# Optimization experiments

Hardware: AMD Instinct MI355X
Metric: run time of the kernel (lower is better)

Reference implementation:

```python
import jax, jax.numpy as jnp
import numpy as np

N_NODES = 100000
N_EDGES = 3200000
IN_F, HID, OUT = 3, 32, 1
NEG_SLOPE = 0.2


def _glorot(key, shape):
    fan_in, fan_out = shape[0], shape[-1]
    lim = jnp.sqrt(6.0 / (fan_in + fan_out)).astype(jnp.float32)
    return jax.random.uniform(key, shape, jnp.float32, -lim, lim)


def setup_inputs() -> dict:
    key = jax.random.key(0)
    ks = jax.random.split(key, 12)
    x = jax.random.normal(ks[0], (N_NODES, IN_F), jnp.float32)
    edge_index = jax.random.randint(ks[1], (2, N_EDGES), 0, N_NODES, jnp.int32)
    return {
        "x": x,
        "edge_index": edge_index,
        "W1": _glorot(ks[2], (IN_F, HID)),
        "att_src1": _glorot(ks[3], (1, HID))[0],
        "att_dst1": _glorot(ks[4], (1, HID))[0],
        "b1": jnp.zeros((HID,), jnp.float32),
        "W2": _glorot(ks[5], (HID, HID)),
        "att_src2": _glorot(ks[6], (1, HID))[0],
        "att_dst2": _glorot(ks[7], (1, HID))[0],
        "b2": jnp.zeros((HID,), jnp.float32),
        "Wl": _glorot(ks[8], (HID, OUT)),
        "bl": jnp.zeros((OUT,), jnp.float32),
    }


def gat_layer(x, src, dst, W, att_src, att_dst, b):
    # h: [N, HID] dense transform
    h = x @ W
    # per-node attention halves (compute once per node, gather per edge)
    a_s = h @ att_src  # [N]
    a_d = h @ att_dst  # [N]
    logits = jax.nn.leaky_relu(a_s[src] + a_d[dst], NEG_SLOPE)  # [E+N]
    # segment-softmax over incoming edges of each dst node
    m = jax.ops.segment_max(logits, dst, num_segments=N_NODES)
    m = jnp.where(jnp.isfinite(m), m, 0.0)
    ex = jnp.exp(logits - m[dst])
    denom = jax.ops.segment_sum(ex, dst, num_segments=N_NODES)
    coef = ex / (denom[dst] + 1e-16)
    # weighted scatter-aggregate of source messages
    out = jax.ops.segment_sum(coef[:, None] * h[src], dst, num_segments=N_NODES)
    return out + b


def reference(x, edge_index, W1, att_src1, att_dst1, b1, W2, att_src2, att_dst2, b2, Wl, bl):
    # PyG GATConv default: add self-loops
    loops = jnp.arange(N_NODES, dtype=edge_index.dtype)
    src = jnp.concatenate([edge_index[0], loops])
    dst = jnp.concatenate([edge_index[1], loops])
    h = gat_layer(x, src, dst, W1, att_src1, att_dst1, b1)
    h = jax.nn.relu(h)  # dropout is identity in eval
    h = gat_layer(h, src, dst, W2, att_src2, att_dst2, b2)
    h = jax.nn.relu(h)
    return h @ Wl + bl
```

## Files before the change

kernel.cpp:

```cpp
#include <hip/hip_runtime.h>
#include <hip/hip_fp16.h>

#define HID 32
#define BN 131
#define NBPAD 768
#define BSTRIDE 4608
#define CHUNK 4096

__device__ __forceinline__ float lrelu(float x) { return x > 0.0f ? x : 0.2f * x; }


struct BinSM {
    int stage[CHUNK];
    unsigned short sbid[CHUNK];
    int lhist[NBPAD], lexcl[NBPAD], lbase[NBPAD], lcur[NBPAD];
    int arr[256];
};
struct AggSM {
    int2  lpair[BSTRIDE];
    int   lhist[256], lscan[256], lcur[256];
    float adT[BN];
};

template<int BLK>
__device__ __forceinline__ void binscatter_chunk(BinSM& S, int base,
        const int* __restrict__ src, const int* __restrict__ dst,
        int* __restrict__ cursor, unsigned int* __restrict__ packed,
        int NBr, int E)
{
    int t = threadIdx.x;
    for (int i = t; i < NBPAD; i += BLK) { S.lhist[i] = 0; S.lcur[i] = 0; }
    __syncthreads();
    int cnt = E - base; if (cnt > CHUNK) cnt = CHUNK;
    for (int i = t; i < cnt; i += BLK)
        atomicAdd(&S.lhist[dst[base + i] / BN], 1);
    __syncthreads();
    int b0 = 3 * t;
    int c0 = 0, c1 = 0, c2 = 0, s = 0;
    if (t < 256) {
        c0 = S.lhist[b0]; c1 = S.lhist[b0 + 1]; c2 = S.lhist[b0 + 2];
        s = c0 + c1 + c2;
        S.arr[t] = s;
    }
    __syncthreads();
    for (int o = 1; o < 256; o <<= 1) {
        int v = (t < 256 && t >= o) ? S.arr[t - o] : 0;
        __syncthreads();
        if (t < 256) S.arr[t] += v;
        __syncthreads();
    }
    if (t < 256) {
        int ex = S.arr[t] - s;
        int e0 = ex, e1 = ex + c0, e2 = ex + c0 + c1;
        S.lexcl[b0] = e0; S.lexcl[b0 + 1] = e1; S.lexcl[b0 + 2] = e2;
        for (int i = 0; i < c0; ++i) S.sbid[e0 + i] = (unsigned short)b0;
        for (int i = 0; i < c1; ++i) S.sbid[e1 + i] = (unsigned short)(b0 + 1);
        for (int i = 0; i < c2; ++i) S.sbid[e2 + i] = (unsigned short)(b0 + 2);
    }
    for (int b = t; b < NBr; b += BLK)
        if (S.lhist[b]) S.lbase[b] = b * BSTRIDE + atomicAdd(&cursor[b], S.lhist[b]);
    __syncthreads();
    for (int i = t; i < cnt; i += BLK) {
        int d = dst[base + i];
        int sv = src[base + i];
        int b = d / BN;
        int dl = d - b * BN;
        int idx = S.lexcl[b] + atomicAdd(&S.lcur[b], 1);
        S.stage[idx] = (int)((unsigned)sv | ((unsigned)dl << 17));
    }
    __syncthreads();
    for (int i = t; i < cnt; i += BLK) {
        int b = S.sbid[i];
        int gpos = S.lbase[b] + (i - S.lexcl[b]);
        if (gpos < (b + 1) * BSTRIDE)
            packed[gpos] = (unsigned)S.stage[i];
    }
}

template<int BLK>
__device__ __forceinline__ void build_csr_pair(int2* lpair, float* adT,
        int* lhist, int* lscan, int* lcur,
        const unsigned int* __restrict__ pk, int cnt,
        const float* __restrict__ a_s, const float* __restrict__ a_d,
        int nodeBase, int N)
{
    int t = threadIdx.x;
    if (t < 256) { lhist[t] = 0; lcur[t] = 0; }
    if (t < BN) { int n = nodeBase + t; adT[t] = (n < N) ? a_d[n] : 0.0f; }
    __syncthreads();
    for (int i = t; i < cnt; i += BLK)
        atomicAdd(&lhist[(pk[i] >> 17) & 255], 1);
    __syncthreads();
    if (t < 256) lscan[t] = lhist[t];
    __syncthreads();
    for (int o = 1; o < 256; o <<= 1) {
        int v = (t < 256 && t >= o) ? lscan[t - o] : 0;
        __syncthreads();
        if (t < 256) lscan[t] += v;
        __syncthreads();
    }
    for (int i = t; i < cnt; i += BLK) {
        unsigned p = pk[i];
        int dl = (p >> 17) & 255;
        int sv = (int)(p & 0x1FFFF);
        float e = __expf(lrelu(a_s[sv] + adT[dl]));
        int pos = atomicAdd(&lcur[dl], 1);
        lpair[(lscan[dl] - lhist[dl]) + pos] = make_int2((int)p, __float_as_int(e));
    }
    __syncthreads();
}

__device__ __forceinline__ void agg_node(const __half* __restrict__ hh,
                                         float ex_self, const float* __restrict__ b,
                                         int n, int f,
                                         const int2* lpair,
                                         int off, int dg, float& vx, float& vy)
{
    float den = ex_self;
    float2 hs = __half22float2(*(const __half2*)(hh + (size_t)n * HID + 2 * f));
    float accx = ex_self * hs.x;
    float accy = ex_self * hs.y;
    int j = 0;
    for (; j + 8 <= dg; j += 8) {
        int2 p0 = lpair[off + j + 0], p1 = lpair[off + j + 1];
        int2 p2 = lpair[off + j + 2], p3 = lpair[off + j + 3];
        int2 p4 = lpair[off + j + 4], p5 = lpair[off + j + 5];
        int2 p6 = lpair[off + j + 6], p7 = lpair[off + j + 7];
        int s0 = p0.x & 0x1FFFF, s1 = p1.x & 0x1FFFF;
        int s2 = p2.x & 0x1FFFF, s3 = p3.x & 0x1FFFF;
        int s4 = p4.x & 0x1FFFF, s5 = p5.x & 0x1FFFF;
        int s6 = p6.x & 0x1FFFF, s7 = p7.x & 0x1FFFF;
        __half2 h0 = *(const __half2*)(hh + (size_t)s0 * HID + 2 * f);
        __half2 h1 = *(const __half2*)(hh + (size_t)s1 * HID + 2 * f);
        __half2 h2 = *(const __half2*)(hh + (size_t)s2 * HID + 2 * f);
        __half2 h3 = *(const __half2*)(hh + (size_t)s3 * HID + 2 * f);
        __half2 h4 = *(const __half2*)(hh + (size_t)s4 * HID + 2 * f);
        __half2 h5 = *(const __half2*)(hh + (size_t)s5 * HID + 2 * f);
        __half2 h6 = *(const __half2*)(hh + (size_t)s6 * HID + 2 * f);
        __half2 h7 = *(const __half2*)(hh + (size_t)s7 * HID + 2 * f);
        float e0 = __int_as_float(p0.y), e1 = __int_as_float(p1.y);
        float e2 = __int_as_float(p2.y), e3 = __int_as_float(p3.y);
        float e4 = __int_as_float(p4.y), e5 = __int_as_float(p5.y);
        float e6 = __int_as_float(p6.y), e7 = __int_as_float(p7.y);
        float2 q0 = __half22float2(h0), q1 = __half22float2(h1);
        float2 q2 = __half22float2(h2), q3 = __half22float2(h3);
        float2 q4 = __half22float2(h4), q5 = __half22float2(h5);
        float2 q6 = __half22float2(h6), q7 = __half22float2(h7);
        den += ((e0 + e1) + (e2 + e3)) + ((e4 + e5) + (e6 + e7));
        accx = fmaf(e0, q0.x, accx); accy = fmaf(e0, q0.y, accy);
        accx = fmaf(e1, q1.x, accx); accy = fmaf(e1, q1.y, accy);
        accx = fmaf(e2, q2.x, accx); accy = fmaf(e2, q2.y, accy);
        accx = fmaf(e3, q3.x, accx); accy = fmaf(e3, q3.y, accy);
        accx = fmaf(e4, q4.x, accx); accy = fmaf(e4, q4.y, accy);
        accx = fmaf(e5, q5.x, accx); accy = fmaf(e5, q5.y, accy);
        accx = fmaf(e6, q6.x, accx); accy = fmaf(e6, q6.y, accy);
        accx = fmaf(e7, q7.x, accx); accy = fmaf(e7, q7.y, accy);
    }
    for (; j < dg; ++j) {
        int2 p0 = lpair[off + j];
        int s0 = p0.x & 0x1FFFF;
        float e0 = __int_as_float(p0.y);
        float2 q0 = __half22float2(*(const __half2*)(hh + (size_t)s0 * HID + 2 * f));
        den += e0;
        accx = fmaf(e0, q0.x, accx);
        accy = fmaf(e0, q0.y, accy);
    }
    float inv = 1.0f / (den + 1e-16f);
    vx = fmaxf(accx * inv + b[2 * f], 0.0f);
    vy = fmaxf(accy * inv + b[2 * f + 1], 0.0f);
}

__device__ __forceinline__ void epi_mid(int n, int f, float vx, float vy,
        const float* __restrict__ W2, const float* __restrict__ as2w,
        const float* __restrict__ ad2w,
        __half* __restrict__ hh_out, float* __restrict__ as_out,
        float* __restrict__ ad_out)
{
    float hx = 0.0f, hy = 0.0f;
    #pragma unroll
    for (int k = 0; k < 16; ++k) {
        float va = __shfl(vx, k, 16);
        float vb = __shfl(vy, k, 16);
        float2 w0 = *(const float2*)(W2 + (2 * k) * HID + 2 * f);
        float2 w1 = *(const float2*)(W2 + (2 * k + 1) * HID + 2 * f);
        hx = fmaf(va, w0.x, hx); hy = fmaf(va, w0.y, hy);
        hx = fmaf(vb, w1.x, hx); hy = fmaf(vb, w1.y, hy);
    }
    *(__half2*)(hh_out + (size_t)n * HID + 2 * f) = __floats2half2_rn(hx, hy);
    float as = hx * as2w[2 * f] + hy * as2w[2 * f + 1];
    float ad = hx * ad2w[2 * f] + hy * ad2w[2 * f + 1];
    #pragma unroll
    for (int m2 = 8; m2 >= 1; m2 >>= 1) {
        as += __shfl_xor(as, m2, 16);
        ad += __shfl_xor(ad, m2, 16);
    }
    if (f == 0) { as_out[n] = as; ad_out[n] = ad; }
}


__global__ void k_transform1(const float* __restrict__ x,
                             const float* __restrict__ W1,
                             const float* __restrict__ att_src,
                             const float* __restrict__ att_dst,
                             __half* __restrict__ hh,
                             float* __restrict__ a_s,
                             float* __restrict__ a_d,
                             int* __restrict__ cursor, int N)
{
    int tid = blockIdx.x * blockDim.x + threadIdx.x;
    if (tid < NBPAD) cursor[tid] = 0;
    int n = tid >> 5, f = tid & 31;
    if (n >= N) return;
    float x0 = x[n * 3 + 0], x1 = x[n * 3 + 1], x2 = x[n * 3 + 2];
    float hv = x0 * W1[f] + x1 * W1[HID + f] + x2 * W1[2 * HID + f];
    hh[(size_t)n * HID + f] = __float2half(hv);
    float as = hv * att_src[f];
    float ad = hv * att_dst[f];
    #pragma unroll
    for (int m = 16; m >= 1; m >>= 1) {
        as += __shfl_xor(as, m, 32);
        ad += __shfl_xor(ad, m, 32);
    }
    if (f == 0) { a_s[n] = as; a_d[n] = ad; }
}

__global__ void __launch_bounds__(512) k_binscatter(const int* __restrict__ src,
        const int* __restrict__ dst, int* __restrict__ cursor,
        unsigned int* __restrict__ packed, int NBr, int E)
{
    __shared__ BinSM S;
    binscatter_chunk<512>(S, blockIdx.x * CHUNK, src, dst, cursor, packed, NBr, E);
}

__global__ void __launch_bounds__(512) k_agg_mid_f(const __half* __restrict__ hh,
        const float* __restrict__ a_s, const float* __restrict__ a_d,
        const int* __restrict__ cursor, const unsigned int* __restrict__ packed,
        const float* __restrict__ b1, const float* __restrict__ W2,
        const float* __restrict__ as2w, const float* __restrict__ ad2w,
        __half* __restrict__ hh_out, float* __restrict__ as_out,
        float* __restrict__ ad_out, int N)
{
    __shared__ AggSM S;
    int bk = blockIdx.x, t = threadIdx.x;
    int cnt = cursor[bk]; if (cnt > BSTRIDE) cnt = BSTRIDE;
    build_csr_pair<512>(S.lpair, S.adT, S.lhist, S.lscan, S.lcur,
                        packed + (size_t)bk * BSTRIDE, cnt, a_s, a_d, bk * BN, N);
    int g = t >> 4, f = t & 15;
    for (int dl = g; dl < BN; dl += 32) {
        int n = bk * BN + dl;
        if (n >= N) continue;
        int off = S.lscan[dl] - S.lhist[dl];
        int dg = S.lhist[dl];
        float exs = __expf(lrelu(a_s[n] + S.adT[dl]));
        float vx, vy;
        agg_node(hh, exs, b1, n, f, S.lpair, off, dg, vx, vy);
        epi_mid(n, f, vx, vy, W2, as2w, ad2w, hh_out, as_out, ad_out);
    }
}

__global__ void __launch_bounds__(512) k_agg_out_f(const __half* __restrict__ hh,
        const float* __restrict__ a_s, const float* __restrict__ a_d,
        const int* __restrict__ cursor, const unsigned int* __restrict__ packed,
        const float* __restrict__ b2, const float* __restrict__ Wl,
        const float* __restrict__ bl, float* __restrict__ out, int N)
{
    __shared__ AggSM S;
    int bk = blockIdx.x, t = threadIdx.x;
    int cnt = cursor[bk]; if (cnt > BSTRIDE) cnt = BSTRIDE;
    build_csr_pair<512>(S.lpair, S.adT, S.lhist, S.lscan, S.lcur,
                        packed + (size_t)bk * BSTRIDE, cnt, a_s, a_d, bk * BN, N);
    int g = t >> 4, f = t & 15;
    for (int dl = g; dl < BN; dl += 32) {
        int n = bk * BN + dl;
        if (n >= N) continue;
        int off = S.lscan[dl] - S.lhist[dl];
        int dg = S.lhist[dl];
        float exs = __expf(lrelu(a_s[n] + S.adT[dl]));
        float vx, vy;
        agg_node(hh, exs, b2, n, f, S.lpair, off, dg, vx, vy);
        float y = vx * Wl[2 * f] + vy * Wl[2 * f + 1];
        #pragma unroll
        for (int m2 = 8; m2 >= 1; m2 >>= 1)
            y += __shfl_xor(y, m2, 16);
        if (f == 0) out[n] = y + bl[0];
    }
}

extern "C" void kernel_launch(void* const* d_in, const int* in_sizes, int n_in,
                              void* d_out, int out_size, void* d_ws, size_t ws_size,
                              hipStream_t stream)
{
    const float* x        = (const float*)d_in[0];
    const int*   eidx     = (const int*)d_in[1];
    const float* W1       = (const float*)d_in[2];
    const float* att_src1 = (const float*)d_in[3];
    const float* att_dst1 = (const float*)d_in[4];
    const float* b1       = (const float*)d_in[5];
    const float* W2       = (const float*)d_in[6];
    const float* att_src2 = (const float*)d_in[7];
    const float* att_dst2 = (const float*)d_in[8];
    const float* b2       = (const float*)d_in[9];
    const float* Wl       = (const float*)d_in[10];
    const float* bl       = (const float*)d_in[11];
    float* out = (float*)d_out;

    int N = in_sizes[0] / 3;
    int E = in_sizes[1] / 2;
    const int* src = eidx;
    const int* dst = eidx + E;
    int NBr = (N + BN - 1) / BN;

    size_t szNHh = (size_t)N * HID * 2;
    size_t szN4  = (size_t)N * 4;
    size_t szPK  = (size_t)NBr * BSTRIDE * 4;

    char* ws = (char*)d_ws;
    __half* h1h    = (__half*)ws; ws += szNHh;
    __half* h2h    = (__half*)ws; ws += szNHh;
    unsigned int* packed = (unsigned int*)ws; ws += szPK;
    float*  a_s1   = (float*)ws;  ws += szN4;
    float*  a_d1   = (float*)ws;  ws += szN4;
    float*  a_s2   = (float*)ws;  ws += szN4;
    float*  a_d2   = (float*)ws;  ws += szN4;
    int*    cursor = (int*)ws;    ws += NBPAD * 4;

    const int B = 256;
    int gridNode32 = (N * HID + B - 1) / B;
    int gridBin    = (E + CHUNK - 1) / CHUNK;

    k_transform1<<<gridNode32, B, 0, stream>>>(x, W1, att_src1, att_dst1,
                                               h1h, a_s1, a_d1, cursor, N);
    k_binscatter<<<gridBin, 512, 0, stream>>>(src, dst, cursor, packed, NBr, E);
    k_agg_mid_f<<<NBr, 512, 0, stream>>>(h1h, a_s1, a_d1, cursor, packed,
                                         b1, W2, att_src2, att_dst2,
                                         h2h, a_s2, a_d2, N);
    k_agg_out_f<<<NBr, 512, 0, stream>>>(h2h, a_s2, a_d2, cursor, packed,
                                         b2, Wl, bl, out, N);
}
```

Measured before the change: 246.4 us.

## Presort edge bins once per dst node and widen aggregation to four features

A new k_sort kernel sorts each bin's packed edges by local destination once and writes per-node offset/degree metadata. Both aggregation passes then only compute edge weights in stream order, with no per-kernel histogram and scan. Bins shrink to 64 nodes with 256-thread blocks, and each thread handles four features using 8-byte half loads. This adds one launch and a global read/write pass over the packed edges in exchange for less repeated shared-memory work and higher occupancy.

```diff
diff --git a/kernel.cpp b/kernel.cpp
--- a/kernel.cpp
+++ b/kernel.cpp
@@ -2,200 +2,14 @@
 #include <hip/hip_fp16.h>
 
 #define HID 32
-#define BN 131
-#define NBPAD 768
-#define BSTRIDE 4608
+#define BN 64
+#define NBPAD 1792
+#define BSTRIDE 2432
 #define CHUNK 4096
+#define EPT 8
+#define SPT 10
 
 __device__ __forceinline__ float lrelu(float x) { return x > 0.0f ? x : 0.2f * x; }
-
-
-struct BinSM {
-    int stage[CHUNK];
-    unsigned short sbid[CHUNK];
-    int lhist[NBPAD], lexcl[NBPAD], lbase[NBPAD], lcur[NBPAD];
-    int arr[256];
-};
-struct AggSM {
-    int2  lpair[BSTRIDE];
-    int   lhist[256], lscan[256], lcur[256];
-    float adT[BN];
-};
-
-template<int BLK>
-__device__ __forceinline__ void binscatter_chunk(BinSM& S, int base,
-        const int* __restrict__ src, const int* __restrict__ dst,
-        int* __restrict__ cursor, unsigned int* __restrict__ packed,
-        int NBr, int E)
-{
-    int t = threadIdx.x;
-    for (int i = t; i < NBPAD; i += BLK) { S.lhist[i] = 0; S.lcur[i] = 0; }
-    __syncthreads();
-    int cnt = E - base; if (cnt > CHUNK) cnt = CHUNK;
-    for (int i = t; i < cnt; i += BLK)
-        atomicAdd(&S.lhist[dst[base + i] / BN], 1);
-    __syncthreads();
-    int b0 = 3 * t;
-    int c0 = 0, c1 = 0, c2 = 0, s = 0;
-    if (t < 256) {
-        c0 = S.lhist[b0]; c1 = S.lhist[b0 + 1]; c2 = S.lhist[b0 + 2];
-        s = c0 + c1 + c2;
-        S.arr[t] = s;
-    }
-    __syncthreads();
-    for (int o = 1; o < 256; o <<= 1) {
-        int v = (t < 256 && t >= o) ? S.arr[t - o] : 0;
-        __syncthreads();
-        if (t < 256) S.arr[t] += v;
-        __syncthreads();
-    }
-    if (t < 256) {
-        int ex = S.arr[t] - s;
-        int e0 = ex, e1 = ex + c0, e2 = ex + c0 + c1;
-        S.lexcl[b0] = e0; S.lexcl[b0 + 1] = e1; S.lexcl[b0 + 2] = e2;
-        for (int i = 0; i < c0; ++i) S.sbid[e0 + i] = (unsigned short)b0;
-        for (int i = 0; i < c1; ++i) S.sbid[e1 + i] = (unsigned short)(b0 + 1);
-        for (int i = 0; i < c2; ++i) S.sbid[e2 + i] = (unsigned short)(b0 + 2);
-    }
-    for (int b = t; b < NBr; b += BLK)
-        if (S.lhist[b]) S.lbase[b] = b * BSTRIDE + atomicAdd(&cursor[b], S.lhist[b]);
-    __syncthreads();
-    for (int i = t; i < cnt; i += BLK) {
-        int d = dst[base + i];
-        int sv = src[base + i];
-        int b = d / BN;
-        int dl = d - b * BN;
-        int idx = S.lexcl[b] + atomicAdd(&S.lcur[b], 1);
-        S.stage[idx] = (int)((unsigned)sv | ((unsigned)dl << 17));
-    }
-    __syncthreads();
-    for (int i = t; i < cnt; i += BLK) {
-        int b = S.sbid[i];
-        int gpos = S.lbase[b] + (i - S.lexcl[b]);
-        if (gpos < (b + 1) * BSTRIDE)
-            packed[gpos] = (unsigned)S.stage[i];
-    }
-}
-
-template<int BLK>
-__device__ __forceinline__ void build_csr_pair(int2* lpair, float* adT,
-        int* lhist, int* lscan, int* lcur,
-        const unsigned int* __restrict__ pk, int cnt,
-        const float* __restrict__ a_s, const float* __restrict__ a_d,
-        int nodeBase, int N)
-{
-    int t = threadIdx.x;
-    if (t < 256) { lhist[t] = 0; lcur[t] = 0; }
-    if (t < BN) { int n = nodeBase + t; adT[t] = (n < N) ? a_d[n] : 0.0f; }
-    __syncthreads();
-    for (int i = t; i < cnt; i += BLK)
-        atomicAdd(&lhist[(pk[i] >> 17) & 255], 1);
-    __syncthreads();
-    if (t < 256) lscan[t] = lhist[t];
-    __syncthreads();
-    for (int o = 1; o < 256; o <<= 1) {
-        int v = (t < 256 && t >= o) ? lscan[t - o] : 0;
-        __syncthreads();
-        if (t < 256) lscan[t] += v;
-        __syncthreads();
-    }
-    for (int i = t; i < cnt; i += BLK) {
-        unsigned p = pk[i];
-        int dl = (p >> 17) & 255;
-        int sv = (int)(p & 0x1FFFF);
-        float e = __expf(lrelu(a_s[sv] + adT[dl]));
-        int pos = atomicAdd(&lcur[dl], 1);
-        lpair[(lscan[dl] - lhist[dl]) + pos] = make_int2((int)p, __float_as_int(e));
-    }
-    __syncthreads();
-}
-
-__device__ __forceinline__ void agg_node(const __half* __restrict__ hh,
-                                         float ex_self, const float* __restrict__ b,
-                                         int n, int f,
-                                         const int2* lpair,
-                                         int off, int dg, float& vx, float& vy)
-{
-    float den = ex_self;
-    float2 hs = __half22float2(*(const __half2*)(hh + (size_t)n * HID + 2 * f));
-    float accx = ex_self * hs.x;
-    float accy = ex_self * hs.y;
-    int j = 0;
-    for (; j + 8 <= dg; j += 8) {
-        int2 p0 = lpair[off + j + 0], p1 = lpair[off + j + 1];
-        int2 p2 = lpair[off + j + 2], p3 = lpair[off + j + 3];
-        int2 p4 = lpair[off + j + 4], p5 = lpair[off + j + 5];
-        int2 p6 = lpair[off + j + 6], p7 = lpair[off + j + 7];
-        int s0 = p0.x & 0x1FFFF, s1 = p1.x & 0x1FFFF;
-        int s2 = p2.x & 0x1FFFF, s3 = p3.x & 0x1FFFF;
-        int s4 = p4.x & 0x1FFFF, s5 = p5.x & 0x1FFFF;
-        int s6 = p6.x & 0x1FFFF, s7 = p7.x & 0x1FFFF;
-        __half2 h0 = *(const __half2*)(hh + (size_t)s0 * HID + 2 * f);
-        __half2 h1 = *(const __half2*)(hh + (size_t)s1 * HID + 2 * f);
-        __half2 h2 = *(const __half2*)(hh + (size_t)s2 * HID + 2 * f);
-        __half2 h3 = *(const __half2*)(hh + (size_t)s3 * HID + 2 * f);
-        __half2 h4 = *(const __half2*)(hh + (size_t)s4 * HID + 2 * f);
-        __half2 h5 = *(const __half2*)(hh + (size_t)s5 * HID + 2 * f);
-        __half2 h6 = *(const __half2*)(hh + (size_t)s6 * HID + 2 * f);
-        __half2 h7 = *(const __half2*)(hh + (size_t)s7 * HID + 2 * f);
-        float e0 = __int_as_float(p0.y), e1 = __int_as_float(p1.y);
-        float e2 = __int_as_float(p2.y), e3 = __int_as_float(p3.y);
-        float e4 = __int_as_float(p4.y), e5 = __int_as_float(p5.y);
-        float e6 = __int_as_float(p6.y), e7 = __int_as_float(p7.y);
-        float2 q0 = __half22float2(h0), q1 = __half22float2(h1);
-        float2 q2 = __half22float2(h2), q3 = __half22float2(h3);
-        float2 q4 = __half22float2(h4), q5 = __half22float2(h5);
-        float2 q6 = __half22float2(h6), q7 = __half22float2(h7);
-        den += ((e0 + e1) + (e2 + e3)) + ((e4 + e5) + (e6 + e7));
-        accx = fmaf(e0, q0.x, accx); accy = fmaf(e0, q0.y, accy);
-        accx = fmaf(e1, q1.x, accx); accy = fmaf(e1, q1.y, accy);
-        accx = fmaf(e2, q2.x, accx); accy = fmaf(e2, q2.y, accy);
-        accx = fmaf(e3, q3.x, accx); accy = fmaf(e3, q3.y, accy);
-        accx = fmaf(e4, q4.x, accx); accy = fmaf(e4, q4.y, accy);
-        accx = fmaf(e5, q5.x, accx); accy = fmaf(e5, q5.y, accy);
-        accx = fmaf(e6, q6.x, accx); accy = fmaf(e6, q6.y, accy);
-        accx = fmaf(e7, q7.x, accx); accy = fmaf(e7, q7.y, accy);
-    }
-    for (; j < dg; ++j) {
-        int2 p0 = lpair[off + j];
-        int s0 = p0.x & 0x1FFFF;
-        float e0 = __int_as_float(p0.y);
-        float2 q0 = __half22float2(*(const __half2*)(hh + (size_t)s0 * HID + 2 * f));
-        den += e0;
-        accx = fmaf(e0, q0.x, accx);
-        accy = fmaf(e0, q0.y, accy);
-    }
-    float inv = 1.0f / (den + 1e-16f);
-    vx = fmaxf(accx * inv + b[2 * f], 0.0f);
-    vy = fmaxf(accy * inv + b[2 * f + 1], 0.0f);
-}
-
-__device__ __forceinline__ void epi_mid(int n, int f, float vx, float vy,
-        const float* __restrict__ W2, const float* __restrict__ as2w,
-        const float* __restrict__ ad2w,
-        __half* __restrict__ hh_out, float* __restrict__ as_out,
-        float* __restrict__ ad_out)
-{
-    float hx = 0.0f, hy = 0.0f;
-    #pragma unroll
-    for (int k = 0; k < 16; ++k) {
-        float va = __shfl(vx, k, 16);
-        float vb = __shfl(vy, k, 16);
-        float2 w0 = *(const float2*)(W2 + (2 * k) * HID + 2 * f);
-        float2 w1 = *(const float2*)(W2 + (2 * k + 1) * HID + 2 * f);
-        hx = fmaf(va, w0.x, hx); hy = fmaf(va, w0.y, hy);
-        hx = fmaf(vb, w1.x, hx); hy = fmaf(vb, w1.y, hy);
-    }
-    *(__half2*)(hh_out + (size_t)n * HID + 2 * f) = __floats2half2_rn(hx, hy);
-    float as = hx * as2w[2 * f] + hy * as2w[2 * f + 1];
-    float ad = hx * ad2w[2 * f] + hy * ad2w[2 * f + 1];
-    #pragma unroll
-    for (int m2 = 8; m2 >= 1; m2 >>= 1) {
-        as += __shfl_xor(as, m2, 16);
-        ad += __shfl_xor(ad, m2, 16);
-    }
-    if (f == 0) { as_out[n] = as; ad_out[n] = ad; }
-}
 
 
 __global__ void k_transform1(const float* __restrict__ x,
@@ -224,17 +38,274 @@
     if (f == 0) { a_s[n] = as; a_d[n] = ad; }
 }
 
+
 __global__ void __launch_bounds__(512) k_binscatter(const int* __restrict__ src,
         const int* __restrict__ dst, int* __restrict__ cursor,
-        unsigned int* __restrict__ packed, int NBr, int E)
-{
-    __shared__ BinSM S;
-    binscatter_chunk<512>(S, blockIdx.x * CHUNK, src, dst, cursor, packed, NBr, E);
-}
-
-__global__ void __launch_bounds__(512) k_agg_mid_f(const __half* __restrict__ hh,
+        unsigned int* __restrict__ packed, int E)
+{
+    __shared__ int stage[CHUNK];
+    __shared__ unsigned short sbid[CHUNK];
+    __shared__ int lidx[NBPAD];
+    __shared__ int lbase[NBPAD];
+    __shared__ int arr[256];
+
+    int t = threadIdx.x;
+    int base = blockIdx.x * CHUNK;
+    int cnt = E - base; if (cnt > CHUNK) cnt = CHUNK;
+
+    for (int i = t; i < NBPAD; i += 512) lidx[i] = 0;
+    __syncthreads();
+
+    int myb[EPT]; unsigned mypk[EPT];
+    #pragma unroll
+    for (int u = 0; u < EPT; ++u) {
+        int i = t + u * 512;
+        myb[u] = -1;
+        if (i < cnt) {
+            int d = dst[base + i];
+            int s = src[base + i];
+            int b = d >> 6;
+            myb[u] = b;
+            mypk[u] = (unsigned)s | ((unsigned)(d & 63) << 17);
+            atomicAdd(&lidx[b], 1);
+        }
+    }
+    __syncthreads();
+
+    int c[7]; int ssum = 0; int b0 = 7 * t;
+    if (t < 256) {
+        #pragma unroll
+        for (int k = 0; k < 7; ++k) { c[k] = lidx[b0 + k]; ssum += c[k]; }
+        arr[t] = ssum;
+    }
+    __syncthreads();
+    for (int o = 1; o < 256; o <<= 1) {
+        int v = (t < 256 && t >= o) ? arr[t - o] : 0;
+        __syncthreads();
+        if (t < 256) arr[t] += v;
+        __syncthreads();
+    }
+    if (t < 256) {
+        int run = arr[t] - ssum;
+        #pragma unroll
+        for (int k = 0; k < 7; ++k) {
+            int ck = c[k];
+            lidx[b0 + k] = run;
+            if (ck) {
+                int gb = (b0 + k) * BSTRIDE + atomicAdd(&cursor[b0 + k], ck);
+                lbase[b0 + k] = gb - run;
+                for (int i2 = 0; i2 < ck; ++i2)
+                    sbid[run + i2] = (unsigned short)(b0 + k);
+            }
+            run += ck;
+        }
+    }
+    __syncthreads();
+
+    #pragma unroll
+    for (int u = 0; u < EPT; ++u) {
+        if (myb[u] >= 0) {
+            int idx = atomicAdd(&lidx[myb[u]], 1);
+            stage[idx] = (int)mypk[u];
+        }
+    }
+    __syncthreads();
+
+    for (int i = t; i < cnt; i += 512) {
+        int b = sbid[i];
+        int gpos = lbase[b] + i;
+        if (gpos < (b + 1) * BSTRIDE) packed[gpos] = (unsigned)stage[i];
+    }
+}
+
+
+__global__ void __launch_bounds__(256) k_sort(const int* __restrict__ cursor,
+        unsigned int* __restrict__ packed, int* __restrict__ nmeta, int N)
+{
+    __shared__ int hist[64];
+    __shared__ int scn[64];
+    __shared__ int stage[BSTRIDE];
+
+    int bk = blockIdx.x, t = threadIdx.x;
+    int cnt = cursor[bk]; if (cnt > BSTRIDE) cnt = BSTRIDE;
+    if (t < 64) hist[t] = 0;
+    __syncthreads();
+
+    unsigned pk[SPT];
+    #pragma unroll
+    for (int u = 0; u < SPT; ++u) {
+        int i = t + u * 256;
+        if (i < cnt) {
+            pk[u] = packed[(size_t)bk * BSTRIDE + i];
+            atomicAdd(&hist[(pk[u] >> 17) & 63], 1);
+        }
+    }
+    __syncthreads();
+
+    if (t < 64) scn[t] = hist[t];
+    __syncthreads();
+    for (int o = 1; o < 64; o <<= 1) {
+        int v = (t < 64 && t >= o) ? scn[t - o] : 0;
+        __syncthreads();
+        if (t < 64) scn[t] += v;
+        __syncthreads();
+    }
+    if (t < 64) {
+        int cdeg = hist[t];
+        int ex = scn[t] - cdeg;
+        hist[t] = ex;
+        int n = bk * BN + t;
+        if (n < N) nmeta[n] = ex | (cdeg << 16);
+    }
+    __syncthreads();
+
+    #pragma unroll
+    for (int u = 0; u < SPT; ++u) {
+        int i = t + u * 256;
+        if (i < cnt) {
+            int idx = atomicAdd(&hist[(pk[u] >> 17) & 63], 1);
+            stage[idx] = (int)pk[u];
+        }
+    }
+    __syncthreads();
+
+    for (int i = t; i < cnt; i += 256)
+        packed[(size_t)bk * BSTRIDE + i] = (unsigned)stage[i];
+}
+
+
+struct AggSM {
+    int2  lpair[BSTRIDE];
+    float adT[BN];
+    float asT[BN];
+    int   meta[BN];
+};
+
+template<int BLK>
+__device__ __forceinline__ void build_stream(AggSM& S,
+        const unsigned int* __restrict__ pk, int cnt,
+        const float* __restrict__ a_s, const float* __restrict__ a_d,
+        const int* __restrict__ nmeta, int nodeBase, int N)
+{
+    int t = threadIdx.x;
+    if (t < BN) {
+        int n = nodeBase + t;
+        bool ok = n < N;
+        S.meta[t] = ok ? nmeta[n] : 0;
+        S.adT[t]  = ok ? a_d[n] : 0.0f;
+        S.asT[t]  = ok ? a_s[n] : 0.0f;
+    }
+    __syncthreads();
+    #pragma unroll
+    for (int u = 0; u < SPT; ++u) {
+        int i = t + u * BLK;
+        if (i < cnt) {
+            unsigned p = pk[i];
+            int sv = (int)(p & 0x1FFFF);
+            int dl = (p >> 17) & 63;
+            float e = __expf(lrelu(a_s[sv] + S.adT[dl]));
+            S.lpair[i] = make_int2(sv, __float_as_int(e));
+        }
+    }
+    __syncthreads();
+}
+
+__device__ __forceinline__ void agg_node8(const __half* __restrict__ hh,
+        float exs, const float* __restrict__ b, int n, int f,
+        const int2* lpair, int off, int dg,
+        float& v0, float& v1, float& v2, float& v3)
+{
+    uint2 us = *(const uint2*)(hh + (size_t)n * HID + 4 * f);
+    float2 s01 = __half22float2(*(__half2*)&us.x);
+    float2 s23 = __half22float2(*(__half2*)&us.y);
+    float den = exs;
+    float a0 = exs * s01.x, a1 = exs * s01.y, a2 = exs * s23.x, a3 = exs * s23.y;
+
+    int j = 0;
+    for (; j + 8 <= dg; j += 8) {
+        int2 p[8]; uint2 uu[8];
+        #pragma unroll
+        for (int q = 0; q < 8; ++q) p[q] = lpair[off + j + q];
+        #pragma unroll
+        for (int q = 0; q < 8; ++q)
+            uu[q] = *(const uint2*)(hh + (size_t)p[q].x * HID + 4 * f);
+        #pragma unroll
+        for (int q = 0; q < 8; ++q) {
+            float e = __int_as_float(p[q].y);
+            float2 qa = __half22float2(*(__half2*)&uu[q].x);
+            float2 qb = __half22float2(*(__half2*)&uu[q].y);
+            den += e;
+            a0 = fmaf(e, qa.x, a0); a1 = fmaf(e, qa.y, a1);
+            a2 = fmaf(e, qb.x, a2); a3 = fmaf(e, qb.y, a3);
+        }
+    }
+    for (; j < dg; ++j) {
+        int2 pp = lpair[off + j];
+        uint2 uu = *(const uint2*)(hh + (size_t)pp.x * HID + 4 * f);
+        float e = __int_as_float(pp.y);
+        float2 qa = __half22float2(*(__half2*)&uu.x);
+        float2 qb = __half22float2(*(__half2*)&uu.y);
+        den += e;
+        a0 = fmaf(e, qa.x, a0); a1 = fmaf(e, qa.y, a1);
+        a2 = fmaf(e, qb.x, a2); a3 = fmaf(e, qb.y, a3);
+    }
+    float inv = 1.0f / (den + 1e-16f);
+    float4 bb = *(const float4*)(b + 4 * f);
+    v0 = fmaxf(a0 * inv + bb.x, 0.0f);
+    v1 = fmaxf(a1 * inv + bb.y, 0.0f);
+    v2 = fmaxf(a2 * inv + bb.z, 0.0f);
+    v3 = fmaxf(a3 * inv + bb.w, 0.0f);
+}
+
+__device__ __forceinline__ void epi_mid8(int n, int f,
+        float v0, float v1, float v2, float v3,
+        const float* __restrict__ W2, const float* __restrict__ as2w,
+        const float* __restrict__ ad2w,
+        __half* __restrict__ hh_out, float* __restrict__ as_out,
+        float* __restrict__ ad_out)
+{
+    float h0 = 0.0f, h1 = 0.0f, h2 = 0.0f, h3 = 0.0f;
+    #pragma unroll
+    for (int k = 0; k < 8; ++k) {
+        float aa[4];
+        aa[0] = __shfl(v0, k, 8);
+        aa[1] = __shfl(v1, k, 8);
+        aa[2] = __shfl(v2, k, 8);
+        aa[3] = __shfl(v3, k, 8);
+        const float* wr = W2 + (4 * k) * HID + 4 * f;
+        #pragma unroll
+        for (int c = 0; c < 4; ++c) {
+            float4 w = *(const float4*)(wr + c * HID);
+            h0 = fmaf(aa[c], w.x, h0);
+            h1 = fmaf(aa[c], w.y, h1);
+            h2 = fmaf(aa[c], w.z, h2);
+            h3 = fmaf(aa[c], w.w, h3);
+        }
+    }
+    __half2 o01 = __floats2half2_rn(h0, h1);
+    __half2 o23 = __floats2half2_rn(h2, h3);
+    uint2 st;
+    st.x = *(unsigned*)&o01;
+    st.y = *(unsigned*)&o23;
+    *(uint2*)(hh_out + (size_t)n * HID + 4 * f) = st;
+
+    float4 asw = *(const float4*)(as2w + 4 * f);
+    float4 adw = *(const float4*)(ad2w + 4 * f);
+    float as = h0 * asw.x + h1 * asw.y + h2 * asw.z + h3 * asw.w;
+    float ad = h0 * adw.x + h1 * adw.y + h2 * adw.z + h3 * adw.w;
+    #pragma unroll
+    for (int m2 = 4; m2 >= 1; m2 >>= 1) {
+        as += __shfl_xor(as, m2, 8);
+        ad += __shfl_xor(ad, m2, 8);
+    }
+    if (f == 0) { as_out[n] = as; ad_out[n] = ad; }
+}
+
+
+__global__ void __launch_bounds__(256, 8) k_agg_mid(const __half* __restrict__ hh,
         const float* __restrict__ a_s, const float* __restrict__ a_d,
         const int* __restrict__ cursor, const unsigned int* __restrict__ packed,
+        const int* __restrict__ nmeta,
         const float* __restrict__ b1, const float* __restrict__ W2,
         const float* __restrict__ as2w, const float* __restrict__ ad2w,
         __half* __restrict__ hh_out, float* __restrict__ as_out,
@@ -243,48 +314,51 @@
     __shared__ AggSM S;
     int bk = blockIdx.x, t = threadIdx.x;
     int cnt = cursor[bk]; if (cnt > BSTRIDE) cnt = BSTRIDE;
-    build_csr_pair<512>(S.lpair, S.adT, S.lhist, S.lscan, S.lcur,
-                        packed + (size_t)bk * BSTRIDE, cnt, a_s, a_d, bk * BN, N);
-    int g = t >> 4, f = t & 15;
+    build_stream<256>(S, packed + (size_t)bk * BSTRIDE, cnt, a_s, a_d,
+                      nmeta, bk * BN, N);
+    int g = t >> 3, f = t & 7;
     for (int dl = g; dl < BN; dl += 32) {
         int n = bk * BN + dl;
         if (n >= N) continue;
-        int off = S.lscan[dl] - S.lhist[dl];
-        int dg = S.lhist[dl];
-        float exs = __expf(lrelu(a_s[n] + S.adT[dl]));
-        float vx, vy;
-        agg_node(hh, exs, b1, n, f, S.lpair, off, dg, vx, vy);
-        epi_mid(n, f, vx, vy, W2, as2w, ad2w, hh_out, as_out, ad_out);
-    }
-}
-
-__global__ void __launch_bounds__(512) k_agg_out_f(const __half* __restrict__ hh,
+        int m = S.meta[dl];
+        int off = m & 0xFFFF, dg = m >> 16;
+        float exs = __expf(lrelu(S.asT[dl] + S.adT[dl]));
+        float v0, v1, v2, v3;
+        agg_node8(hh, exs, b1, n, f, S.lpair, off, dg, v0, v1, v2, v3);
+        epi_mid8(n, f, v0, v1, v2, v3, W2, as2w, ad2w, hh_out, as_out, ad_out);
+    }
+}
+
+__global__ void __launch_bounds__(256, 8) k_agg_out(const __half* __restrict__ hh,
         const float* __restrict__ a_s, const float* __restrict__ a_d,
         const int* __restrict__ cursor, const unsigned int* __restrict__ packed,
+        const int* __restrict__ nmeta,
         const float* __restrict__ b2, const float* __restrict__ Wl,
         const float* __restrict__ bl, float* __restrict__ out, int N)
 {
     __shared__ AggSM S;
     int bk = blockIdx.x, t = threadIdx.x;
     int cnt = cursor[bk]; if (cnt > BSTRIDE) cnt = BSTRIDE;
-    build_csr_pair<512>(S.lpair, S.adT, S.lhist, S.lscan, S.lcur,
-                        packed + (size_t)bk * BSTRIDE, cnt, a_s, a_d, bk * BN, N);
-    int g = t >> 4, f = t & 15;
+    build_stream<256>(S, packed + (size_t)bk * BSTRIDE, cnt, a_s, a_d,
+                      nmeta, bk * BN, N);
+    int g = t >> 3, f = t & 7;
     for (int dl = g; dl < BN; dl += 32) {
         int n = bk * BN + dl;
         if (n >= N) continue;
-        int off = S.lscan[dl] - S.lhist[dl];
-        int dg = S.lhist[dl];
-        float exs = __expf(lrelu(a_s[n] + S.adT[dl]));
-        float vx, vy;
-        agg_node(hh, exs, b2, n, f, S.lpair, off, dg, vx, vy);
-        float y = vx * Wl[2 * f] + vy * Wl[2 * f + 1];
-        #pragma unroll
-        for (int m2 = 8; m2 >= 1; m2 >>= 1)
-            y += __shfl_xor(y, m2, 16);
+        int m = S.meta[dl];
+        int off = m & 0xFFFF, dg = m >> 16;
+        float exs = __expf(lrelu(S.asT[dl] + S.adT[dl]));
+        float v0, v1, v2, v3;
+        agg_node8(hh, exs, b2, n, f, S.lpair, off, dg, v0, v1, v2, v3);
+        float4 wl = *(const float4*)(Wl + 4 * f);
+        float y = v0 * wl.x + v1 * wl.y + v2 * wl.z + v3 * wl.w;
+        #pragma unroll
+        for (int m2 = 4; m2 >= 1; m2 >>= 1)
+            y += __shfl_xor(y, m2, 8);
         if (f == 0) out[n] = y + bl[0];
     }
 }
+
 
 extern "C" void kernel_launch(void* const* d_in, const int* in_sizes, int n_in,
                               void* d_out, int out_size, void* d_ws, size_t ws_size,
@@ -322,6 +396,7 @@
     float*  a_d1   = (float*)ws;  ws += szN4;
     float*  a_s2   = (float*)ws;  ws += szN4;
     float*  a_d2   = (float*)ws;  ws += szN4;
+    int*    nmeta  = (int*)ws;    ws += szN4;
     int*    cursor = (int*)ws;    ws += NBPAD * 4;
 
     const int B = 256;
@@ -330,10 +405,11 @@
 
     k_transform1<<<gridNode32, B, 0, stream>>>(x, W1, att_src1, att_dst1,
                                                h1h, a_s1, a_d1, cursor, N);
-    k_binscatter<<<gridBin, 512, 0, stream>>>(src, dst, cursor, packed, NBr, E);
-    k_agg_mid_f<<<NBr, 512, 0, stream>>>(h1h, a_s1, a_d1, cursor, packed,
-                                         b1, W2, att_src2, att_dst2,
-                                         h2h, a_s2, a_d2, N);
-    k_agg_out_f<<<NBr, 512, 0, stream>>>(h2h, a_s2, a_d2, cursor, packed,
-                                         b2, Wl, bl, out, N);
-}
+    k_binscatter<<<gridBin, 512, 0, stream>>>(src, dst, cursor, packed, E);
+    k_sort<<<NBr, 256, 0, stream>>>(cursor, packed, nmeta, N);
+    k_agg_mid<<<NBr, 256, 0, stream>>>(h1h, a_s1, a_d1, cursor, packed, nmeta,
+                                       b1, W2, att_src2, att_dst2,
+                                       h2h, a_s2, a_d2, N);
+    k_agg_out<<<NBr, 256, 0, stream>>>(h2h, a_s2, a_d2, cursor, packed, nmeta,
+                                       b2, Wl, bl, out, N);
+}
```

After: 322.4 us. 1.31x slower.

## Split aggregation bins across three blocks and register-cache binscatter edges

Applied to the files above, without the earlier changes.

Each aggregation block now handles a third of a destination bin, about 44 nodes, at 256 threads, with a much smaller shared CSR buffer. This raises occupancy and the number of blocks, but each block rescans the whole bin's packed edges and filters them, so the packed edge reads triple. The binscatter kernel uses larger chunks, keeps each thread's src/dst in registers instead of reading them twice, and pads the global cursors to avoid contention on shared cache lines. The lpair entries now store a plain source index, which removes the masking in the gather loop, and a capacity clamp (LPCAP) could drop edges for very high-degree slices.

```diff
diff --git a/kernel.cpp b/kernel.cpp
--- a/kernel.cpp
+++ b/kernel.cpp
@@ -5,9 +5,41 @@
 #define BN 131
 #define NBPAD 768
 #define BSTRIDE 4608
-#define CHUNK 4096
+#define CHUNK 6144
+#define EPT 12
+#define CPAD 16
+#define NSPLIT 3
+#define HNMAX 44
+#define LPCAP 1700
 
 __device__ __forceinline__ float lrelu(float x) { return x > 0.0f ? x : 0.2f * x; }
+
+
+__global__ void k_transform1(const float* __restrict__ x,
+                             const float* __restrict__ W1,
+                             const float* __restrict__ att_src,
+                             const float* __restrict__ att_dst,
+                             __half* __restrict__ hh,
+                             float* __restrict__ a_s,
+                             float* __restrict__ a_d,
+                             int* __restrict__ cursor, int N)
+{
+    int tid = blockIdx.x * blockDim.x + threadIdx.x;
+    if (tid < NBPAD * CPAD) cursor[tid] = 0;
+    int n = tid >> 5, f = tid & 31;
+    if (n >= N) return;
+    float x0 = x[n * 3 + 0], x1 = x[n * 3 + 1], x2 = x[n * 3 + 2];
+    float hv = x0 * W1[f] + x1 * W1[HID + f] + x2 * W1[2 * HID + f];
+    hh[(size_t)n * HID + f] = __float2half(hv);
+    float as = hv * att_src[f];
+    float ad = hv * att_dst[f];
+    #pragma unroll
+    for (int m = 16; m >= 1; m >>= 1) {
+        as += __shfl_xor(as, m, 32);
+        ad += __shfl_xor(ad, m, 32);
+    }
+    if (f == 0) { a_s[n] = as; a_d[n] = ad; }
+}
 
 
 struct BinSM {
@@ -16,25 +48,31 @@
     int lhist[NBPAD], lexcl[NBPAD], lbase[NBPAD], lcur[NBPAD];
     int arr[256];
 };
-struct AggSM {
-    int2  lpair[BSTRIDE];
-    int   lhist[256], lscan[256], lcur[256];
-    float adT[BN];
-};
-
-template<int BLK>
-__device__ __forceinline__ void binscatter_chunk(BinSM& S, int base,
-        const int* __restrict__ src, const int* __restrict__ dst,
-        int* __restrict__ cursor, unsigned int* __restrict__ packed,
-        int NBr, int E)
-{
+
+__global__ void __launch_bounds__(512) k_binscatter(const int* __restrict__ src,
+        const int* __restrict__ dst, int* __restrict__ cursor,
+        unsigned int* __restrict__ packed, int NBr, int E)
+{
+    __shared__ BinSM S;
     int t = threadIdx.x;
-    for (int i = t; i < NBPAD; i += BLK) { S.lhist[i] = 0; S.lcur[i] = 0; }
-    __syncthreads();
+    int base = blockIdx.x * CHUNK;
     int cnt = E - base; if (cnt > CHUNK) cnt = CHUNK;
-    for (int i = t; i < cnt; i += BLK)
-        atomicAdd(&S.lhist[dst[base + i] / BN], 1);
-    __syncthreads();
+
+    for (int i = t; i < NBPAD; i += 512) { S.lhist[i] = 0; S.lcur[i] = 0; }
+    __syncthreads();
+
+    int myd[EPT], mys[EPT];
+    #pragma unroll
+    for (int u = 0; u < EPT; ++u) {
+        int i = t + u * 512;
+        myd[u] = -1;
+        if (i < cnt) { myd[u] = dst[base + i]; mys[u] = src[base + i]; }
+    }
+    #pragma unroll
+    for (int u = 0; u < EPT; ++u)
+        if (myd[u] >= 0) atomicAdd(&S.lhist[myd[u] / BN], 1);
+    __syncthreads();
+
     int b0 = 3 * t;
     int c0 = 0, c1 = 0, c2 = 0, s = 0;
     if (t < 256) {
@@ -57,19 +95,24 @@
         for (int i = 0; i < c1; ++i) S.sbid[e1 + i] = (unsigned short)(b0 + 1);
         for (int i = 0; i < c2; ++i) S.sbid[e2 + i] = (unsigned short)(b0 + 2);
     }
-    for (int b = t; b < NBr; b += BLK)
-        if (S.lhist[b]) S.lbase[b] = b * BSTRIDE + atomicAdd(&cursor[b], S.lhist[b]);
-    __syncthreads();
-    for (int i = t; i < cnt; i += BLK) {
-        int d = dst[base + i];
-        int sv = src[base + i];
-        int b = d / BN;
-        int dl = d - b * BN;
-        int idx = S.lexcl[b] + atomicAdd(&S.lcur[b], 1);
-        S.stage[idx] = (int)((unsigned)sv | ((unsigned)dl << 17));
-    }
-    __syncthreads();
-    for (int i = t; i < cnt; i += BLK) {
+    for (int b = t; b < NBr; b += 512)
+        if (S.lhist[b])
+            S.lbase[b] = b * BSTRIDE + atomicAdd(&cursor[b * CPAD], S.lhist[b]);
+    __syncthreads();
+
+    #pragma unroll
+    for (int u = 0; u < EPT; ++u) {
+        if (myd[u] >= 0) {
+            int d = myd[u];
+            int b = d / BN;
+            int dl = d - b * BN;
+            int idx = S.lexcl[b] + atomicAdd(&S.lcur[b], 1);
+            S.stage[idx] = (int)((unsigned)mys[u] | ((unsigned)dl << 17));
+        }
+    }
+    __syncthreads();
+
+    for (int i = t; i < cnt; i += 512) {
         int b = S.sbid[i];
         int gpos = S.lbase[b] + (i - S.lexcl[b]);
         if (gpos < (b + 1) * BSTRIDE)
@@ -77,35 +120,45 @@
     }
 }
 
-template<int BLK>
-__device__ __forceinline__ void build_csr_pair(int2* lpair, float* adT,
-        int* lhist, int* lscan, int* lcur,
+
+struct AggSM {
+    int2  lpair[LPCAP];
+    int   hist[64], scn[64], cur[64];
+    float adT[HNMAX];
+};
+
+__device__ __forceinline__ void build_slice(AggSM& S,
         const unsigned int* __restrict__ pk, int cnt,
         const float* __restrict__ a_s, const float* __restrict__ a_d,
-        int nodeBase, int N)
+        int nodeBase, int dlo, int HN, int N)
 {
     int t = threadIdx.x;
-    if (t < 256) { lhist[t] = 0; lcur[t] = 0; }
-    if (t < BN) { int n = nodeBase + t; adT[t] = (n < N) ? a_d[n] : 0.0f; }
-    __syncthreads();
-    for (int i = t; i < cnt; i += BLK)
-        atomicAdd(&lhist[(pk[i] >> 17) & 255], 1);
-    __syncthreads();
-    if (t < 256) lscan[t] = lhist[t];
-    __syncthreads();
-    for (int o = 1; o < 256; o <<= 1) {
-        int v = (t < 256 && t >= o) ? lscan[t - o] : 0;
+    if (t < 64) { S.hist[t] = 0; S.cur[t] = 0; }
+    if (t < HN) { int n = nodeBase + dlo + t; S.adT[t] = (n < N) ? a_d[n] : 0.0f; }
+    __syncthreads();
+    for (int i = t; i < cnt; i += 256) {
+        unsigned ldl = ((pk[i] >> 17) & 255) - (unsigned)dlo;
+        if (ldl < (unsigned)HN) atomicAdd(&S.hist[ldl], 1);
+    }
+    __syncthreads();
+    if (t < 64) S.scn[t] = S.hist[t];
+    __syncthreads();
+    for (int o = 1; o < 64; o <<= 1) {
+        int v = (t < 64 && t >= o) ? S.scn[t - o] : 0;
         __syncthreads();
-        if (t < 256) lscan[t] += v;
+        if (t < 64) S.scn[t] += v;
         __syncthreads();
     }
-    for (int i = t; i < cnt; i += BLK) {
+    for (int i = t; i < cnt; i += 256) {
         unsigned p = pk[i];
-        int dl = (p >> 17) & 255;
-        int sv = (int)(p & 0x1FFFF);
-        float e = __expf(lrelu(a_s[sv] + adT[dl]));
-        int pos = atomicAdd(&lcur[dl], 1);
-        lpair[(lscan[dl] - lhist[dl]) + pos] = make_int2((int)p, __float_as_int(e));
+        unsigned ldl = ((p >> 17) & 255) - (unsigned)dlo;
+        if (ldl < (unsigned)HN) {
+            int sv = (int)(p & 0x1FFFF);
+            float e = __expf(lrelu(a_s[sv] + S.adT[ldl]));
+            int pos = atomicAdd(&S.cur[ldl], 1);
+            int idx = (S.scn[ldl] - S.hist[ldl]) + pos;
+            if (idx < LPCAP) S.lpair[idx] = make_int2(sv, __float_as_int(e));
+        }
     }
     __syncthreads();
 }
@@ -126,18 +179,14 @@
         int2 p2 = lpair[off + j + 2], p3 = lpair[off + j + 3];
         int2 p4 = lpair[off + j + 4], p5 = lpair[off + j + 5];
         int2 p6 = lpair[off + j + 6], p7 = lpair[off + j + 7];
-        int s0 = p0.x & 0x1FFFF, s1 = p1.x & 0x1FFFF;
-        int s2 = p2.x & 0x1FFFF, s3 = p3.x & 0x1FFFF;
-        int s4 = p4.x & 0x1FFFF, s5 = p5.x & 0x1FFFF;
-        int s6 = p6.x & 0x1FFFF, s7 = p7.x & 0x1FFFF;
-        __half2 h0 = *(const __half2*)(hh + (size_t)s0 * HID + 2 * f);
-        __half2 h1 = *(const __half2*)(hh + (size_t)s1 * HID + 2 * f);
-        __half2 h2 = *(const __half2*)(hh + (size_t)s2 * HID + 2 * f);
-        __half2 h3 = *(const __half2*)(hh + (size_t)s3 * HID + 2 * f);
-        __half2 h4 = *(const __half2*)(hh + (size_t)s4 * HID + 2 * f);
-        __half2 h5 = *(const __half2*)(hh + (size_t)s5 * HID + 2 * f);
-        __half2 h6 = *(const __half2*)(hh + (size_t)s6 * HID + 2 * f);
-        __half2 h7 = *(const __half2*)(hh + (size_t)s7 * HID + 2 * f);
+        __half2 h0 = *(const __half2*)(hh + (size_t)p0.x * HID + 2 * f);
+        __half2 h1 = *(const __half2*)(hh + (size_t)p1.x * HID + 2 * f);
+        __half2 h2 = *(const __half2*)(hh + (size_t)p2.x * HID + 2 * f);
+        __half2 h3 = *(const __half2*)(hh + (size_t)p3.x * HID + 2 * f);
+        __half2 h4 = *(const __half2*)(hh + (size_t)p4.x * HID + 2 * f);
+        __half2 h5 = *(const __half2*)(hh + (size_t)p5.x * HID + 2 * f);
+        __half2 h6 = *(const __half2*)(hh + (size_t)p6.x * HID + 2 * f);
+        __half2 h7 = *(const __half2*)(hh + (size_t)p7.x * HID + 2 * f);
         float e0 = __int_as_float(p0.y), e1 = __int_as_float(p1.y);
         float e2 = __int_as_float(p2.y), e3 = __int_as_float(p3.y);
         float e4 = __int_as_float(p4.y), e5 = __int_as_float(p5.y);
@@ -158,9 +207,8 @@
     }
     for (; j < dg; ++j) {
         int2 p0 = lpair[off + j];
-        int s0 = p0.x & 0x1FFFF;
         float e0 = __int_as_float(p0.y);
-        float2 q0 = __half22float2(*(const __half2*)(hh + (size_t)s0 * HID + 2 * f));
+        float2 q0 = __half22float2(*(const __half2*)(hh + (size_t)p0.x * HID + 2 * f));
         den += e0;
         accx = fmaf(e0, q0.x, accx);
         accy = fmaf(e0, q0.y, accy);
@@ -198,41 +246,7 @@
 }
 
 
-__global__ void k_transform1(const float* __restrict__ x,
-                             const float* __restrict__ W1,
-                             const float* __restrict__ att_src,
-                             const float* __restrict__ att_dst,
-                             __half* __restrict__ hh,
-                             float* __restrict__ a_s,
-                             float* __restrict__ a_d,
-                             int* __restrict__ cursor, int N)
-{
-    int tid = blockIdx.x * blockDim.x + threadIdx.x;
-    if (tid < NBPAD) cursor[tid] = 0;
-    int n = tid >> 5, f = tid & 31;
-    if (n >= N) return;
-    float x0 = x[n * 3 + 0], x1 = x[n * 3 + 1], x2 = x[n * 3 + 2];
-    float hv = x0 * W1[f] + x1 * W1[HID + f] + x2 * W1[2 * HID + f];
-    hh[(size_t)n * HID + f] = __float2half(hv);
-    float as = hv * att_src[f];
-    float ad = hv * att_dst[f];
-    #pragma unroll
-    for (int m = 16; m >= 1; m >>= 1) {
-        as += __shfl_xor(as, m, 32);
-        ad += __shfl_xor(ad, m, 32);
-    }
-    if (f == 0) { a_s[n] = as; a_d[n] = ad; }
-}
-
-__global__ void __launch_bounds__(512) k_binscatter(const int* __restrict__ src,
-        const int* __restrict__ dst, int* __restrict__ cursor,
-        unsigned int* __restrict__ packed, int NBr, int E)
-{
-    __shared__ BinSM S;
-    binscatter_chunk<512>(S, blockIdx.x * CHUNK, src, dst, cursor, packed, NBr, E);
-}
-
-__global__ void __launch_bounds__(512) k_agg_mid_f(const __half* __restrict__ hh,
+__global__ void __launch_bounds__(256, 8) k_agg_mid(const __half* __restrict__ hh,
         const float* __restrict__ a_s, const float* __restrict__ a_d,
         const int* __restrict__ cursor, const unsigned int* __restrict__ packed,
         const float* __restrict__ b1, const float* __restrict__ W2,
@@ -241,41 +255,47 @@
         float* __restrict__ ad_out, int N)
 {
     __shared__ AggSM S;
-    int bk = blockIdx.x, t = threadIdx.x;
-    int cnt = cursor[bk]; if (cnt > BSTRIDE) cnt = BSTRIDE;
-    build_csr_pair<512>(S.lpair, S.adT, S.lhist, S.lscan, S.lcur,
-                        packed + (size_t)bk * BSTRIDE, cnt, a_s, a_d, bk * BN, N);
+    int bid = blockIdx.x, t = threadIdx.x;
+    int bk = bid / NSPLIT, k = bid - NSPLIT * bk;
+    int dlo = k * HNMAX;
+    int HN = BN - dlo; if (HN > HNMAX) HN = HNMAX;
+    int cnt = cursor[bk * CPAD]; if (cnt > BSTRIDE) cnt = BSTRIDE;
+    build_slice(S, packed + (size_t)bk * BSTRIDE, cnt, a_s, a_d, bk * BN, dlo, HN, N);
     int g = t >> 4, f = t & 15;
-    for (int dl = g; dl < BN; dl += 32) {
-        int n = bk * BN + dl;
+    for (int ldl = g; ldl < HN; ldl += 16) {
+        int n = bk * BN + dlo + ldl;
         if (n >= N) continue;
-        int off = S.lscan[dl] - S.lhist[dl];
-        int dg = S.lhist[dl];
-        float exs = __expf(lrelu(a_s[n] + S.adT[dl]));
+        int off = S.scn[ldl] - S.hist[ldl];
+        int dg = S.hist[ldl];
+        if (off + dg > LPCAP) dg = LPCAP - off;
+        float exs = __expf(lrelu(a_s[n] + S.adT[ldl]));
         float vx, vy;
         agg_node(hh, exs, b1, n, f, S.lpair, off, dg, vx, vy);
         epi_mid(n, f, vx, vy, W2, as2w, ad2w, hh_out, as_out, ad_out);
     }
 }
 
-__global__ void __launch_bounds__(512) k_agg_out_f(const __half* __restrict__ hh,
+__global__ void __launch_bounds__(256, 8) k_agg_out(const __half* __restrict__ hh,
         const float* __restrict__ a_s, const float* __restrict__ a_d,
         const int* __restrict__ cursor, const unsigned int* __restrict__ packed,
         const float* __restrict__ b2, const float* __restrict__ Wl,
         const float* __restrict__ bl, float* __restrict__ out, int N)
 {
     __shared__ AggSM S;
-    int bk = blockIdx.x, t = threadIdx.x;
-    int cnt = cursor[bk]; if (cnt > BSTRIDE) cnt = BSTRIDE;
-    build_csr_pair<512>(S.lpair, S.adT, S.lhist, S.lscan, S.lcur,
-                        packed + (size_t)bk * BSTRIDE, cnt, a_s, a_d, bk * BN, N);
+    int bid = blockIdx.x, t = threadIdx.x;
+    int bk = bid / NSPLIT, k = bid - NSPLIT * bk;
+    int dlo = k * HNMAX;
+    int HN = BN - dlo; if (HN > HNMAX) HN = HNMAX;
+    int cnt = cursor[bk * CPAD]; if (cnt > BSTRIDE) cnt = BSTRIDE;
+    build_slice(S, packed + (size_t)bk * BSTRIDE, cnt, a_s, a_d, bk * BN, dlo, HN, N);
     int g = t >> 4, f = t & 15;
-    for (int dl = g; dl < BN; dl += 32) {
-        int n = bk * BN + dl;
+    for (int ldl = g; ldl < HN; ldl += 16) {
+        int n = bk * BN + dlo + ldl;
         if (n >= N) continue;
-        int off = S.lscan[dl] - S.lhist[dl];
-        int dg = S.lhist[dl];
-        float exs = __expf(lrelu(a_s[n] + S.adT[dl]));
+        int off = S.scn[ldl] - S.hist[ldl];
+        int dg = S.hist[ldl];
+        if (off + dg > LPCAP) dg = LPCAP - off;
+        float exs = __expf(lrelu(a_s[n] + S.adT[ldl]));
         float vx, vy;
         agg_node(hh, exs, b2, n, f, S.lpair, off, dg, vx, vy);
         float y = vx * Wl[2 * f] + vy * Wl[2 * f + 1];
@@ -285,6 +305,7 @@
         if (f == 0) out[n] = y + bl[0];
     }
 }
+
 
 extern "C" void kernel_launch(void* const* d_in, const int* in_sizes, int n_in,
                               void* d_out, int out_size, void* d_ws, size_t ws_size,
@@ -322,18 +343,19 @@
     float*  a_d1   = (float*)ws;  ws += szN4;
     float*  a_s2   = (float*)ws;  ws += szN4;
     float*  a_d2   = (float*)ws;  ws += szN4;
-    int*    cursor = (int*)ws;    ws += NBPAD * 4;
+    int*    cursor = (int*)ws;    ws += (size_t)NBPAD * CPAD * 4;
 
     const int B = 256;
     int gridNode32 = (N * HID + B - 1) / B;
     int gridBin    = (E + CHUNK - 1) / CHUNK;
+    int gridAgg    = NBr * NSPLIT;
 
     k_transform1<<<gridNode32, B, 0, stream>>>(x, W1, att_src1, att_dst1,
                                                h1h, a_s1, a_d1, cursor, N);
     k_binscatter<<<gridBin, 512, 0, stream>>>(src, dst, cursor, packed, NBr, E);
-    k_agg_mid_f<<<NBr, 512, 0, stream>>>(h1h, a_s1, a_d1, cursor, packed,
-                                         b1, W2, att_src2, att_dst2,
-                                         h2h, a_s2, a_d2, N);
-    k_agg_out_f<<<NBr, 512, 0, stream>>>(h2h, a_s2, a_d2, cursor, packed,
-                                         b2, Wl, bl, out, N);
-}
+    k_agg_mid<<<gridAgg, 256, 0, stream>>>(h1h, a_s1, a_d1, cursor, packed,
+                                           b1, W2, att_src2, att_dst2,
+                                           h2h, a_s2, a_d2, N);
+    k_agg_out<<<gridAgg, 256, 0, stream>>>(h2h, a_s2, a_d2, cursor, packed,
+                                           b2, Wl, bl, out, N);
+}
```

Result: slower. 288.3 us (+17.0%).
